# Kernel tuning notes

Measured on AMD Instinct MI355X. Metric: run time of the kernel, lower is better.

## Reference

```python
import jax, jax.numpy as jnp
import numpy as np

B, F, N, J, L_LAYERS = 16, 16, 1024, 8, 3


def setup_inputs() -> dict:
    key = jax.random.key(0)
    k1, k2, k3 = jax.random.split(key, 3)
    x = jax.random.normal(k1, (B, F, N), dtype=jnp.float32)
    psi = jax.random.normal(k2, (J, N, N), dtype=jnp.float32) / np.sqrt(N)
    lowpass = jax.random.uniform(k3, (N,), dtype=jnp.float32) / N
    return {"x": x, "psi": psi, "lowpass": lowpass, "L": L_LAYERS}


def reference(x, psi, lowpass, L):
    # x: [B, F, N] graph signals; psi: [J, N, N] wavelet filterbank; lowpass: [N]
    Bs, Fs, Ns = x.shape
    # layer-0 lowpass projection: phi = x @ lowpass -> [B, F, 1]
    phi = jnp.einsum('bfn,n->bf', x, lowpass)[:, :, None]
    S_x = x[:, None, :, :]  # [B, K=1, F, N]
    for _ in range(1, L):
        # apply all J wavelets to all K branches, then abs nonlinearity
        # (branch order k-major, j-minor matches the torch cat loop)
        S_x = jnp.abs(jnp.einsum('bkfn,jnm->bkjfm', S_x, psi))
        K = S_x.shape[1] * S_x.shape[2]
        S_x = S_x.reshape(Bs, K, Fs, Ns)
        # lowpass-pool every branch: [B, F, K]
        phi_l = jnp.einsum('bkfn,n->bfk', S_x, lowpass)
        phi = jnp.concatenate([phi, phi_l], axis=2)
    return phi  # [B, F, 1 + J + J^2 + ... + J^(L-1)]
```

## Files before the change

kernel.cpp:

```cpp
#include <hip/hip_runtime.h>

#define ND 1024
#define NNE (ND*ND)

typedef float f32x4 __attribute__((ext_vector_type(4)));
typedef int i32x4 __attribute__((ext_vector_type(4)));
typedef int i32x8 __attribute__((ext_vector_type(8)));

__device__ __forceinline__ void gload_lds16(const void* g, void* l) {
  __builtin_amdgcn_global_load_lds(
      (const __attribute__((address_space(1))) void*)g,
      (__attribute__((address_space(3))) void*)l, 16, 0, 0);
}

__global__ void convert_phi0_kernel(const float* __restrict__ x, const float* __restrict__ lp,
                                    unsigned char* __restrict__ x8, float* __restrict__ phi) {
  __shared__ float ws[4];
  int row = blockIdx.x;
  int t   = threadIdx.x;
  if (t >= 1 && t < 73) phi[row * 73 + t] = 0.f;
  float4 v = reinterpret_cast<const float4*>(x + (size_t)row * ND)[t];
  float4 l = reinterpret_cast<const float4*>(lp)[t];
  int pk = __builtin_amdgcn_cvt_pk_fp8_f32(v.x, v.y, 0, false);
  pk = __builtin_amdgcn_cvt_pk_fp8_f32(v.z, v.w, pk, true);
  reinterpret_cast<unsigned int*>(x8 + (size_t)row * ND)[t] = (unsigned int)pk;
  float s = v.x * l.x + v.y * l.y + v.z * l.z + v.w * l.w;
  #pragma unroll
  for (int off = 32; off; off >>= 1) s += __shfl_xor(s, off);
  if ((t & 63) == 0) ws[t >> 6] = s;
  __syncthreads();
  if (t == 0) phi[row * 73] = ws[0] + ws[1] + ws[2] + ws[3];
}

__global__ void psi_transpose_kernel(const float* __restrict__ psi,
                                     unsigned char* __restrict__ out8) {
  __shared__ float t[32][33];
  int blk = blockIdx.x;
  int j  = blk >> 10;
  int tn = (blk >> 5) & 31;
  int tm = blk & 31;
  const float* src = psi + ((size_t)j << 20) + (size_t)(tn << 5) * ND + (tm << 5);
  int r  = threadIdx.x >> 3;
  int c4 = (threadIdx.x & 7) << 2;
  float4 v = *reinterpret_cast<const float4*>(src + (size_t)r * ND + c4);
  t[r][c4 + 0] = v.x; t[r][c4 + 1] = v.y; t[r][c4 + 2] = v.z; t[r][c4 + 3] = v.w;
  __syncthreads();
  float f0 = t[c4 + 0][r], f1 = t[c4 + 1][r], f2 = t[c4 + 2][r], f3 = t[c4 + 3][r];
  size_t base = ((size_t)j << 20) + (size_t)((tm << 5) + r) * ND + (tn << 5) + c4;
  int pk = __builtin_amdgcn_cvt_pk_fp8_f32(f0, f1, 0, false);
  pk = __builtin_amdgcn_cvt_pk_fp8_f32(f2, f3, pk, true);
  *reinterpret_cast<unsigned int*>(out8 + base) = (unsigned int)pk;
}

__device__ __forceinline__ i32x8 dsr_frag8(const unsigned char* base, int r, int l4) {
  int s0 = l4 * 2;
  i32x4 lo = *reinterpret_cast<const i32x4*>(base + r * 128 + ((s0 ^ (r & 7)) << 4));
  i32x4 hi = *reinterpret_cast<const i32x4*>(base + r * 128 + (((s0 + 1) ^ (r & 7)) << 4));
  return __builtin_shufflevector(lo, hi, 0, 1, 2, 3, 4, 5, 6, 7);
}

__global__ __launch_bounds__(256, 2)
void gemm8_l1(const unsigned char* __restrict__ A,
              const unsigned char* __restrict__ BT,
              const float* __restrict__ lowpass,
              unsigned char* __restrict__ Sout,
              float* __restrict__ phi) {
  __shared__ __align__(16) unsigned char As[128 * 128];
  __shared__ __align__(16) unsigned char Bs[128 * 128];

  const int tid  = threadIdx.x;
  const int lane = tid & 63;
  const int w    = tid >> 6;
  const int wrow = w >> 1, wcol = w & 1;
  const int l15  = lane & 15, l4 = lane >> 4;

  const int wg = blockIdx.x;
  const int j  = wg & 7;
  const int t  = wg >> 3;
  const int mtile = t & 1, ntile = t >> 1;
  const int row0 = mtile * 128, n0 = ntile * 128;
  const unsigned char* Bj = BT + (size_t)j * NNE;

  f32x4 acc[4][4] = {};

  #pragma unroll 1
  for (int k0 = 0; k0 < ND; k0 += 128) {
    __syncthreads();
    #pragma unroll
    for (int p = 0; p < 4; ++p) {
      int c = p * 256 + tid;
      int r = c >> 3;
      int s = (c & 7) ^ (r & 7);
      gload_lds16(A + (size_t)(row0 + r) * ND + k0 + (s << 4), As + c * 16);
    }
    #pragma unroll
    for (int p = 0; p < 4; ++p) {
      int c = p * 256 + tid;
      int r = c >> 3;
      int s = (c & 7) ^ (r & 7);
      gload_lds16(Bj + (size_t)(n0 + r) * ND + k0 + (s << 4), Bs + c * 16);
    }
    __syncthreads();

    i32x8 a[4], b[4];
    #pragma unroll
    for (int m = 0; m < 4; ++m)
      a[m] = dsr_frag8(As, wrow * 64 + m * 16 + l15, l4);
    #pragma unroll
    for (int n = 0; n < 4; ++n)
      b[n] = dsr_frag8(Bs, wcol * 64 + n * 16 + l15, l4);
    #pragma unroll
    for (int m = 0; m < 4; ++m)
      #pragma unroll
      for (int n = 0; n < 4; ++n)
        acc[m][n] = __builtin_amdgcn_mfma_scale_f32_16x16x128_f8f6f4(
            a[m], b[n], acc[m][n], 0, 0, 0, 0x7f7f7f7f, 0, 0x7f7f7f7f);
  }

  float lp[4];
  #pragma unroll
  for (int n = 0; n < 4; ++n)
    lp[n] = lowpass[n0 + wcol * 64 + n * 16 + l15];

  #pragma unroll
  for (int m = 0; m < 4; ++m) {
    #pragma unroll
    for (int r = 0; r < 4; ++r) {
      int rg = row0 + wrow * 64 + m * 16 + l4 * 4 + r;
      float psum = 0.f;
      #pragma unroll
      for (int n = 0; n < 4; ++n) {
        float v = fabsf(acc[m][n][r]);
        psum += v * lp[n];
        int colg = n0 + wcol * 64 + n * 16 + l15;
        size_t si = ((size_t)((rg >> 4) * 8 + j) * 16 + (rg & 15)) * ND + colg;
        int pk = __builtin_amdgcn_cvt_pk_fp8_f32(v, v, 0, false);
        Sout[si] = (unsigned char)(pk & 0xff);
      }
      psum += __shfl_xor(psum, 1);
      psum += __shfl_xor(psum, 2);
      psum += __shfl_xor(psum, 4);
      psum += __shfl_xor(psum, 8);
      if (l15 == 0) {
        int pidx = rg * 73 + 1 + j;
        atomicAdd(&phi[pidx], psum);
      }
    }
  }
}

__global__ __launch_bounds__(256, 2)
void gemm8_l2(const unsigned char* __restrict__ A,
              const unsigned char* __restrict__ BT,
              const float* __restrict__ lowpass,
              float* __restrict__ phi) {
  __shared__ __align__(16) unsigned char As[128 * 128];
  __shared__ __align__(16) unsigned char Bs[128 * 128];

  const int tid  = threadIdx.x;
  const int lane = tid & 63;
  const int w    = tid >> 6;
  const int wrow = w >> 1, wcol = w & 1;
  const int l15  = lane & 15, l4 = lane >> 4;

  const int wg  = blockIdx.x;
  const int j   = wg & 7;
  const int idx = wg >> 3;
  const unsigned char* Bj = BT + (size_t)j * NNE;

  #pragma unroll 1
  for (int tt = 0; tt < 2; ++tt) {
    const int t = idx + tt * 64;
    const int mtile = t & 15, ntile = t >> 4;
    const int row0 = mtile * 128, n0 = ntile * 128;

    f32x4 acc[4][4] = {};

    #pragma unroll 1
    for (int k0 = 0; k0 < ND; k0 += 128) {
      __syncthreads();
      #pragma unroll
      for (int p = 0; p < 4; ++p) {
        int c = p * 256 + tid;
        int r = c >> 3;
        int s = (c & 7) ^ (r & 7);
        gload_lds16(A + (size_t)(row0 + r) * ND + k0 + (s << 4), As + c * 16);
      }
      #pragma unroll
      for (int p = 0; p < 4; ++p) {
        int c = p * 256 + tid;
        int r = c >> 3;
        int s = (c & 7) ^ (r & 7);
        gload_lds16(Bj + (size_t)(n0 + r) * ND + k0 + (s << 4), Bs + c * 16);
      }
      __syncthreads();

      i32x8 a[4], b[4];
      #pragma unroll
      for (int m = 0; m < 4; ++m)
        a[m] = dsr_frag8(As, wrow * 64 + m * 16 + l15, l4);
      #pragma unroll
      for (int n = 0; n < 4; ++n)
        b[n] = dsr_frag8(Bs, wcol * 64 + n * 16 + l15, l4);
      #pragma unroll
      for (int m = 0; m < 4; ++m)
        #pragma unroll
        for (int n = 0; n < 4; ++n)
          acc[m][n] = __builtin_amdgcn_mfma_scale_f32_16x16x128_f8f6f4(
              a[m], b[n], acc[m][n], 0, 0, 0, 0x7f7f7f7f, 0, 0x7f7f7f7f);
    }

    float lp[4];
    #pragma unroll
    for (int n = 0; n < 4; ++n)
      lp[n] = lowpass[n0 + wcol * 64 + n * 16 + l15];

    #pragma unroll
    for (int m = 0; m < 4; ++m) {
      #pragma unroll
      for (int r = 0; r < 4; ++r) {
        int rg = row0 + wrow * 64 + m * 16 + l4 * 4 + r;
        float psum = 0.f;
        #pragma unroll
        for (int n = 0; n < 4; ++n)
          psum += fabsf(acc[m][n][r]) * lp[n];
        psum += __shfl_xor(psum, 1);
        psum += __shfl_xor(psum, 2);
        psum += __shfl_xor(psum, 4);
        psum += __shfl_xor(psum, 8);
        if (l15 == 0) {
          int pidx = ((rg >> 7) * 16 + (rg & 15)) * 73 + 9 + ((rg >> 4) & 7) * 8 + j;
          atomicAdd(&phi[pidx], psum);
        }
      }
    }
  }
}

extern "C" void kernel_launch(void* const* d_in, const int* in_sizes, int n_in,
                              void* d_out, int out_size, void* d_ws, size_t ws_size,
                              hipStream_t stream) {
  (void)in_sizes; (void)n_in; (void)ws_size; (void)out_size;
  const float* x       = (const float*)d_in[0];
  const float* psi     = (const float*)d_in[1];
  const float* lowpass = (const float*)d_in[2];
  float* phi = (float*)d_out;

  unsigned char* x8    = (unsigned char*)d_ws;
  unsigned char* psiT8 = (unsigned char*)((char*)d_ws + (1u << 20));
  unsigned char* S1f8  = (unsigned char*)((char*)d_ws + (10u << 20));

  convert_phi0_kernel<<<256, 256, 0, stream>>>(x, lowpass, x8, phi);
  psi_transpose_kernel<<<8192, 256, 0, stream>>>(psi, psiT8);

  gemm8_l1<<<128, 256, 0, stream>>>(x8, psiT8, lowpass, S1f8, phi);

  gemm8_l2<<<512, 256, 0, stream>>>(S1f8, psiT8, lowpass, phi);
}
```

Before: 64.63 us.

## Merge x conversion and psi fp8 transpose into one prep kernel with larger tiles

Result: no change. 64.37 us (-0.4%).

```diff
diff --git a/kernel.cpp b/kernel.cpp
--- a/kernel.cpp
+++ b/kernel.cpp
@@ -13,43 +13,62 @@
       (__attribute__((address_space(3))) void*)l, 16, 0, 0);
 }
 
-__global__ void convert_phi0_kernel(const float* __restrict__ x, const float* __restrict__ lp,
-                                    unsigned char* __restrict__ x8, float* __restrict__ phi) {
+__global__ __launch_bounds__(256)
+void prep_kernel(const float* __restrict__ psi, unsigned char* __restrict__ out8,
+                 const float* __restrict__ x, const float* __restrict__ lp,
+                 unsigned char* __restrict__ x8, float* __restrict__ phi) {
+  __shared__ __align__(16) unsigned char T[128 * 144];
   __shared__ float ws[4];
-  int row = blockIdx.x;
-  int t   = threadIdx.x;
-  if (t >= 1 && t < 73) phi[row * 73 + t] = 0.f;
-  float4 v = reinterpret_cast<const float4*>(x + (size_t)row * ND)[t];
-  float4 l = reinterpret_cast<const float4*>(lp)[t];
-  int pk = __builtin_amdgcn_cvt_pk_fp8_f32(v.x, v.y, 0, false);
-  pk = __builtin_amdgcn_cvt_pk_fp8_f32(v.z, v.w, pk, true);
-  reinterpret_cast<unsigned int*>(x8 + (size_t)row * ND)[t] = (unsigned int)pk;
-  float s = v.x * l.x + v.y * l.y + v.z * l.z + v.w * l.w;
-  #pragma unroll
-  for (int off = 32; off; off >>= 1) s += __shfl_xor(s, off);
-  if ((t & 63) == 0) ws[t >> 6] = s;
+  const int blk = blockIdx.x;
+  const int tid = threadIdx.x;
+
+  if (blk >= 512) {
+    int row = blk - 512;
+    if (tid >= 1 && tid < 73) phi[row * 73 + tid] = 0.f;
+    float4 v = reinterpret_cast<const float4*>(x + (size_t)row * ND)[tid];
+    float4 l = reinterpret_cast<const float4*>(lp)[tid];
+    int pk = __builtin_amdgcn_cvt_pk_fp8_f32(v.x, v.y, 0, false);
+    pk = __builtin_amdgcn_cvt_pk_fp8_f32(v.z, v.w, pk, true);
+    reinterpret_cast<unsigned int*>(x8 + (size_t)row * ND)[tid] = (unsigned int)pk;
+    float s = v.x * l.x + v.y * l.y + v.z * l.z + v.w * l.w;
+    #pragma unroll
+    for (int off = 32; off; off >>= 1) s += __shfl_xor(s, off);
+    if ((tid & 63) == 0) ws[tid >> 6] = s;
+    __syncthreads();
+    if (tid == 0) phi[row * 73] = ws[0] + ws[1] + ws[2] + ws[3];
+    return;
+  }
+
+  const int j  = blk >> 6;
+  const int t6 = blk & 63;
+  const int tn = t6 >> 3, tm = t6 & 7;
+  const int n0 = tn * 128, m0 = tm * 128;
+  const float* src = psi + ((size_t)j << 20) + (size_t)n0 * ND + m0;
+
+  const int rgrp = tid >> 5;
+  const int c4   = (tid & 31) << 2;
+  #pragma unroll
+  for (int it = 0; it < 16; ++it) {
+    int nl = it * 8 + rgrp;
+    float4 v = *reinterpret_cast<const float4*>(src + (size_t)nl * ND + c4);
+    int p01 = __builtin_amdgcn_cvt_pk_fp8_f32(v.x, v.y, 0, false);
+    int p23 = __builtin_amdgcn_cvt_pk_fp8_f32(v.z, v.w, 0, false);
+    T[(c4 + 0) * 144 + nl] = (unsigned char)(p01 & 0xff);
+    T[(c4 + 1) * 144 + nl] = (unsigned char)((p01 >> 8) & 0xff);
+    T[(c4 + 2) * 144 + nl] = (unsigned char)(p23 & 0xff);
+    T[(c4 + 3) * 144 + nl] = (unsigned char)((p23 >> 8) & 0xff);
+  }
   __syncthreads();
-  if (t == 0) phi[row * 73] = ws[0] + ws[1] + ws[2] + ws[3];
-}
-
-__global__ void psi_transpose_kernel(const float* __restrict__ psi,
-                                     unsigned char* __restrict__ out8) {
-  __shared__ float t[32][33];
-  int blk = blockIdx.x;
-  int j  = blk >> 10;
-  int tn = (blk >> 5) & 31;
-  int tm = blk & 31;
-  const float* src = psi + ((size_t)j << 20) + (size_t)(tn << 5) * ND + (tm << 5);
-  int r  = threadIdx.x >> 3;
-  int c4 = (threadIdx.x & 7) << 2;
-  float4 v = *reinterpret_cast<const float4*>(src + (size_t)r * ND + c4);
-  t[r][c4 + 0] = v.x; t[r][c4 + 1] = v.y; t[r][c4 + 2] = v.z; t[r][c4 + 3] = v.w;
-  __syncthreads();
-  float f0 = t[c4 + 0][r], f1 = t[c4 + 1][r], f2 = t[c4 + 2][r], f3 = t[c4 + 3][r];
-  size_t base = ((size_t)j << 20) + (size_t)((tm << 5) + r) * ND + (tn << 5) + c4;
-  int pk = __builtin_amdgcn_cvt_pk_fp8_f32(f0, f1, 0, false);
-  pk = __builtin_amdgcn_cvt_pk_fp8_f32(f2, f3, pk, true);
-  *reinterpret_cast<unsigned int*>(out8 + base) = (unsigned int)pk;
+
+  unsigned char* dst = out8 + ((size_t)j << 20) + (size_t)m0 * ND + n0;
+  const int mrow = tid >> 3;
+  const int ch   = (tid & 7) << 4;
+  #pragma unroll
+  for (int it = 0; it < 4; ++it) {
+    int ml = it * 32 + mrow;
+    uint4 v = *reinterpret_cast<const uint4*>(&T[ml * 144 + ch]);
+    *reinterpret_cast<uint4*>(dst + (size_t)ml * ND + ch) = v;
+  }
 }
 
 __device__ __forceinline__ i32x8 dsr_frag8(const unsigned char* base, int r, int l4) {
@@ -250,8 +269,7 @@
   unsigned char* psiT8 = (unsigned char*)((char*)d_ws + (1u << 20));
   unsigned char* S1f8  = (unsigned char*)((char*)d_ws + (10u << 20));
 
-  convert_phi0_kernel<<<256, 256, 0, stream>>>(x, lowpass, x8, phi);
-  psi_transpose_kernel<<<8192, 256, 0, stream>>>(psi, psiT8);
+  prep_kernel<<<768, 256, 0, stream>>>(psi, psiT8, x, lowpass, x8, phi);
 
   gemm8_l1<<<128, 256, 0, stream>>>(x8, psiT8, lowpass, S1f8, phi);
 
```
